# Performance work log

Hardware: AMD Instinct MI355X
Metric: run time of the kernel (lower is better)

Reference implementation:

```python
import jax, jax.numpy as jnp
import numpy as np

DIM = 192
HEADS = 6
HEAD_DIM = DIM // HEADS          # 32
N_WIN_TOK = 2 * 6 * 12           # 144 tokens per (2,6,12) window
BIAS_ROWS = (2 * 12 - 1) * 6 * 6 * 2 * 2  # 3312
N_WINDOWS = 960


def setup_inputs() -> dict:
    key = jax.random.key(0)
    ks = jax.random.split(key, 8)
    x = jax.random.normal(ks[0], (N_WINDOWS, N_WIN_TOK, DIM), dtype=jnp.float32)
    mask = jax.random.randint(ks[1], (N_WINDOWS, N_WIN_TOK, N_WIN_TOK), 0, 2, dtype=jnp.int32)
    rel_index = jax.random.randint(ks[2], (N_WIN_TOK, N_WIN_TOK), 0, BIAS_ROWS, dtype=jnp.int32)
    # parameters (torch nn.Linear equivalents, stored as [in, out])
    w_qkv = jax.random.normal(ks[3], (DIM, 3 * DIM), dtype=jnp.float32) * 0.02
    b_qkv = jnp.zeros((3 * DIM,), dtype=jnp.float32)
    w_out = jax.random.normal(ks[4], (DIM, DIM), dtype=jnp.float32) * 0.02
    b_out = jnp.zeros((DIM,), dtype=jnp.float32)
    bias_table = jax.random.normal(ks[5], (BIAS_ROWS, HEADS), dtype=jnp.float32) * 0.02
    return {"x": x, "mask": mask, "rel_index": rel_index,
            "w_qkv": w_qkv, "b_qkv": b_qkv, "w_out": w_out, "b_out": b_out,
            "bias_table": bias_table}


def reference(x, mask, rel_index, w_qkv, b_qkv, w_out, b_out, bias_table):
    nW, N, dim = x.shape
    scale = jnp.asarray(HEAD_DIM, x.dtype) ** -0.5
    # qkv projection: [nW, N, 3, heads, head_dim]
    qkv = (x @ w_qkv + b_qkv).reshape(nW, N, 3, HEADS, HEAD_DIM)
    q, k, v = qkv[:, :, 0], qkv[:, :, 1], qkv[:, :, 2]   # each [nW, N, heads, hd]
    # attention scores [nW, heads, N, N]
    attn = jnp.einsum('wnhd,wmhd->whnm', q * scale, k)
    # relative-position bias gather: table[rel_index] -> [N, N, heads] -> [heads, N, N]
    bias = bias_table[rel_index].transpose(2, 0, 1)
    attn = attn + bias[None]
    # additive mask: positions where mask == 0 get -1e9
    attn = jnp.where(mask[:, None, :, :] == 0, jnp.asarray(-1e9, attn.dtype), attn)
    attn = jax.nn.softmax(attn, axis=-1)
    out = jnp.einsum('whnm,wmhd->wnhd', attn, v).reshape(nW, N, dim)
    return out @ w_out + b_out
```

## Files before the change

### kernel.cpp

```cpp
#include <hip/hip_runtime.h>
#include <math.h>

#define NW 960
#define NT 144
#define DIM 192
#define NH 6
#define HD 32
#define WCOLS 576

typedef __bf16 bf16x8 __attribute__((ext_vector_type(8)));
typedef float floatx4 __attribute__((ext_vector_type(4)));

__device__ __forceinline__ unsigned short f2bf(float x) {
    union { float f; unsigned u; } v; v.f = x;
    unsigned r = v.u + 0x7fffu + ((v.u >> 16) & 1u);
    return (unsigned short)(r >> 16);
}
__device__ __forceinline__ float bf2f(unsigned short b) {
    union { unsigned u; float f; } v; v.u = ((unsigned)b) << 16;
    return v.f;
}
__device__ __forceinline__ floatx4 mfma16(bf16x8 a, bf16x8 b, floatx4 c) {
    return __builtin_amdgcn_mfma_f32_16x16x32_bf16(a, b, c, 0, 0, 0);
}
__device__ __forceinline__ bf16x8 lds_ld8(const unsigned short* p) {
    bf16x8 v;
    __builtin_memcpy(&v, p, 16);
    return v;
}

__global__ void prep_bias(const int* __restrict__ rel_index,
                          const float* __restrict__ bias_table,
                          float* __restrict__ bias_pre) {
    int i = blockIdx.x * 256 + threadIdx.x;
    if (i < NH * NT * NT) {
        int h = i / (NT * NT);
        int rem = i - h * (NT * NT);
        bias_pre[i] = bias_table[rel_index[rem] * NH + h];
    }
}

__global__ void prep_wq_frag(const float* __restrict__ w_qkv,
                             unsigned short* __restrict__ wh,
                             unsigned short* __restrict__ wl) {
    int i = blockIdx.x * 256 + threadIdx.x;
    if (i < NH * 6 * 6 * 512) {
        int h = i / 18432; int r = i - h * 18432;
        int j = r / 3072;  r -= j * 3072;
        int kt = r / 512;  r -= kt * 512;
        int lane = r >> 3, pos = r & 7;
        int col96 = j * 16 + (lane & 15);
        int k = kt * 32 + (lane >> 4) * 8 + pos;
        float v = w_qkv[k * WCOLS + (col96 >> 5) * DIM + h * HD + (col96 & 31)];
        unsigned short hi = f2bf(v);
        wh[i] = hi;
        wl[i] = f2bf(v - bf2f(hi));
    }
}

__global__ void prep_wo_frag(const float* __restrict__ w_out,
                             unsigned short* __restrict__ wh,
                             unsigned short* __restrict__ wl) {
    int i = blockIdx.x * 256 + threadIdx.x;
    if (i < 12 * 6 * 512) {
        int nt = i / 3072; int r = i - nt * 3072;
        int kt = r / 512;  r -= kt * 512;
        int lane = r >> 3, pos = r & 7;
        int ocol = nt * 16 + (lane & 15);
        int k = kt * 32 + (lane >> 4) * 8 + pos;
        float v = w_out[k * DIM + ocol];
        unsigned short hi = f2bf(v);
        wh[i] = hi;
        wl[i] = f2bf(v - bf2f(hi));
    }
}

__global__ __launch_bounds__(768, 3)
void fused(const float* __restrict__ x, const int* __restrict__ mask,
           const float* __restrict__ bias_pre,
           const unsigned short* __restrict__ wqh, const unsigned short* __restrict__ wql,
           const float* __restrict__ b_qkv,
           const unsigned short* __restrict__ woh_g, const unsigned short* __restrict__ wol_g,
           const float* __restrict__ b_out, float* __restrict__ out)
{
    __shared__ __align__(16) unsigned short lds[63904];
    const int XFo = 0, Q2o = 27648, K2o = 36864, V2o = 46080, Po = 56320, MBo = 62464;

    const int t = threadIdx.x;
    const int w = blockIdx.x;
    const int lane = t & 63, wv = t >> 6;
    const int c = lane & 15, q = lane >> 4;
    const float scale = 0.17677669529663687f;
    const float* xg = x + (size_t)w * NT * DIM;

    {
        unsigned* XFd = (unsigned*)&lds[XFo];
        #pragma unroll
        for (int l = 0; l < 18; ++l) {
            int d = t + l * 768;
            int kt = d / 2304; int r2 = d - kt * 2304;
            int tile = r2 >> 8; int r3 = r2 & 255;
            int ln = r3 >> 2, pp = r3 & 3;
            int n = tile * 16 + (ln & 15);
            int k = kt * 32 + (ln >> 4) * 8 + pp * 2;
            float2 xv = *(const float2*)&xg[n * DIM + k];
            XFd[d] = (unsigned)f2bf(xv.x) | ((unsigned)f2bf(xv.y) << 16);
        }
    }
    for (int e = t; e < 1024; e += 768) {
        int gi = e >> 8, l2 = 32 + ((e >> 3) & 31), pos = e & 7;
        lds[V2o + (gi * 5 + 4) * 512 + l2 * 8 + pos] = 0;
    }
    {
        unsigned* mb = (unsigned*)&lds[MBo];
        #pragma unroll 4
        for (int rr = 0; rr < 12; ++rr) {
            int n = wv * 12 + rr;
            const int* mrow = mask + ((size_t)w * NT + n) * NT;
            unsigned long long b0 = __ballot(mrow[lane] != 0);
            unsigned long long b1 = __ballot(mrow[64 + lane] != 0);
            int mv = (lane < 16) ? mrow[128 + lane] : 0;
            unsigned long long b2 = __ballot(mv != 0);
            if (lane == 0) {
                mb[n * 5 + 0] = (unsigned)b0;
                mb[n * 5 + 1] = (unsigned)(b0 >> 32);
                mb[n * 5 + 2] = (unsigned)b1;
                mb[n * 5 + 3] = (unsigned)(b1 >> 32);
                mb[n * 5 + 4] = (unsigned)b2;
            }
        }
    }

    const int hl   = wv / 6;
    const int j6   = wv % 6;
    const int part = j6 >> 1;
    const int jj   = j6 & 1;
    const int hl2  = wv & 1;
    const int sA   = wv >> 1;

    floatx4 Oacc[3][2][2];

    auto attn_unit = [&](int g, int s, floatx4* O) {
        const int hB = 2 * g + hl2;
        float bb[4][9];
        const float* bbase = bias_pre + hB * (NT * NT) + (s * 16 + q * 4) * NT + c;
        #pragma unroll
        for (int r = 0; r < 4; ++r)
            #pragma unroll
            for (int nt = 0; nt < 9; ++nt)
                bb[r][nt] = bbase[r * NT + nt * 16];
        bf16x8 qf = *(const bf16x8*)&lds[Q2o + (hl2 * 9 + s) * 512 + lane * 8];
        floatx4 sacc[9];
        __builtin_amdgcn_s_setprio(1);
        #pragma unroll
        for (int nt = 0; nt < 9; ++nt) {
            bf16x8 kf = *(const bf16x8*)&lds[K2o + (hl2 * 9 + nt) * 512 + lane * 8];
            sacc[nt] = mfma16(qf, kf, (floatx4)0.0f);
        }
        __builtin_amdgcn_s_setprio(0);
        const unsigned* mb = (const unsigned*)&lds[MBo];
        unsigned mwv[4][5];
        #pragma unroll
        for (int r = 0; r < 4; ++r) {
            int n = s * 16 + q * 4 + r;
            #pragma unroll
            for (int k5 = 0; k5 < 5; ++k5) mwv[r][k5] = mb[n * 5 + k5];
        }
        float e[4][9], mx[4];
        #pragma unroll
        for (int r = 0; r < 4; ++r) mx[r] = -1e30f;
        #pragma unroll
        for (int r = 0; r < 4; ++r)
            #pragma unroll
            for (int nt = 0; nt < 9; ++nt) {
                float val = sacc[nt][r] + bb[r][nt];
                unsigned bit = (mwv[r][nt >> 1] >> (((nt & 1) << 4) + c)) & 1u;
                val = bit ? val : -1e9f;
                e[r][nt] = val; mx[r] = fmaxf(mx[r], val);
            }
        #pragma unroll
        for (int o = 8; o; o >>= 1)
            #pragma unroll
            for (int r = 0; r < 4; ++r) mx[r] = fmaxf(mx[r], __shfl_xor(mx[r], o, 64));
        float sum[4] = {0.f, 0.f, 0.f, 0.f};
        #pragma unroll
        for (int r = 0; r < 4; ++r)
            #pragma unroll
            for (int nt = 0; nt < 9; ++nt) { e[r][nt] = __expf(e[r][nt] - mx[r]); sum[r] += e[r][nt]; }
        #pragma unroll
        for (int o = 8; o; o >>= 1)
            #pragma unroll
            for (int r = 0; r < 4; ++r) sum[r] += __shfl_xor(sum[r], o, 64);
        float rinv[4];
        #pragma unroll
        for (int r = 0; r < 4; ++r) rinv[r] = 1.0f / sum[r];
        floatx4 o0 = (floatx4)0.0f, o1 = (floatx4)0.0f;
        unsigned short* pbase = &lds[Po + wv * 512];
        #pragma unroll
        for (int sl = 0; sl < 5; ++sl) {
            asm volatile("" ::: "memory");
            #pragma unroll
            for (int r = 0; r < 4; ++r)
                #pragma unroll
                for (int ntl = 0; ntl < 2; ++ntl) {
                    int nt = 2 * sl + ntl;
                    unsigned short pv = 0;
                    if (nt < 9) pv = f2bf(e[r][nt] * rinv[r]);
                    pbase[((q * 4 + r) + 16 * ((ntl << 1) + (c >> 3))) * 8 + (c & 7)] = pv;
                }
            asm volatile("" ::: "memory");
            bf16x8 pf = lds_ld8(&pbase[lane * 8]);
            __builtin_amdgcn_s_setprio(1);
            o0 = mfma16(pf, *(const bf16x8*)&lds[V2o + ((hl2 * 2 + 0) * 5 + sl) * 512 + lane * 8], o0);
            o1 = mfma16(pf, *(const bf16x8*)&lds[V2o + ((hl2 * 2 + 1) * 5 + sl) * 512 + lane * 8], o1);
            __builtin_amdgcn_s_setprio(0);
        }
        O[0] = o0; O[1] = o1;
    };

    #pragma unroll
    for (int g = 0; g < 3; ++g) {
        __syncthreads();
        const int hg = 2 * g + hl;

        const unsigned short* bhp = wqh + (size_t)((hg * 6 + j6) * 6) * 512 + lane * 8;
        const unsigned short* blp = wql + (size_t)((hg * 6 + j6) * 6) * 512 + lane * 8;
        bf16x8 bh[6], bl[6];
        #pragma unroll
        for (int kt = 0; kt < 6; ++kt) {
            bh[kt] = *(const bf16x8*)&bhp[kt * 512];
            bl[kt] = *(const bf16x8*)&blp[kt * 512];
        }
        float bq = b_qkv[part * DIM + hg * HD + jj * 16 + c];

        #pragma unroll
        for (int i3 = 0; i3 < 3; ++i3) {
            floatx4 a[3];
            #pragma unroll
            for (int ii = 0; ii < 3; ++ii) a[ii] = (floatx4)0.0f;
            __builtin_amdgcn_s_setprio(1);
            #pragma unroll
            for (int kt = 0; kt < 6; ++kt) {
                #pragma unroll
                for (int ii = 0; ii < 3; ++ii) {
                    bf16x8 ah = *(const bf16x8*)&lds[XFo + (kt * 9 + i3 * 3 + ii) * 512 + lane * 8];
                    a[ii] = mfma16(ah, bh[kt], a[ii]);
                    a[ii] = mfma16(ah, bl[kt], a[ii]);
                }
            }
            __builtin_amdgcn_s_setprio(0);
            #pragma unroll
            for (int ii = 0; ii < 3; ++ii) {
                int i = i3 * 3 + ii;
                #pragma unroll
                for (int r = 0; r < 4; ++r) {
                    float v = a[ii][r] + bq;
                    int col32 = jj * 16 + c;
                    if (part == 0) {
                        lds[Q2o + (hl * 9 + i) * 512 + ((q * 4 + r) + 16 * (col32 >> 3)) * 8 + (col32 & 7)] = f2bf(v * scale);
                    } else if (part == 1) {
                        lds[K2o + (hl * 9 + i) * 512 + ((q * 4 + r) + 16 * (col32 >> 3)) * 8 + (col32 & 7)] = f2bf(v);
                    } else {
                        int n = i * 16 + q * 4 + r;
                        lds[V2o + ((hl * 2 + jj) * 5 + (n >> 5)) * 512 + (c + 16 * ((n >> 3) & 3)) * 8 + (n & 7)] = f2bf(v);
                    }
                }
            }
        }
        __syncthreads();

        attn_unit(g, sA, Oacc[g][0]);
        if (wv < 6) attn_unit(g, 6 + sA, Oacc[g][1]);
    }

    #pragma unroll
    for (int g = 0; g < 3; ++g) {
        int hB = 2 * g + hl2;
        #pragma unroll
        for (int ntv = 0; ntv < 2; ++ntv)
            #pragma unroll
            for (int r = 0; r < 4; ++r)
                lds[XFo + (hB * 9 + sA) * 512 +
                    ((q * 4 + r) + 16 * (ntv * 2 + (c >> 3))) * 8 + (c & 7)] =
                    f2bf(Oacc[g][0][ntv][r]);
        if (wv < 6) {
            #pragma unroll
            for (int ntv = 0; ntv < 2; ++ntv)
                #pragma unroll
                for (int r = 0; r < 4; ++r)
                    lds[XFo + (hB * 9 + 6 + sA) * 512 +
                        ((q * 4 + r) + 16 * (ntv * 2 + (c >> 3))) * 8 + (c & 7)] =
                        f2bf(Oacc[g][1][ntv][r]);
        }
    }
    __syncthreads();

    {
        const unsigned short* whp = woh_g + (size_t)(wv * 6) * 512 + lane * 8;
        const unsigned short* wlp = wol_g + (size_t)(wv * 6) * 512 + lane * 8;
        bf16x8 wh[6], wlo[6];
        #pragma unroll
        for (int kt = 0; kt < 6; ++kt) {
            wh[kt]  = *(const bf16x8*)&whp[kt * 512];
            wlo[kt] = *(const bf16x8*)&wlp[kt * 512];
        }
        float bo = b_out[wv * 16 + c];
        #pragma unroll
        for (int i3 = 0; i3 < 3; ++i3) {
            floatx4 a2[3];
            #pragma unroll
            for (int ii = 0; ii < 3; ++ii) a2[ii] = (floatx4)0.0f;
            __builtin_amdgcn_s_setprio(1);
            #pragma unroll
            for (int kt = 0; kt < 6; ++kt) {
                #pragma unroll
                for (int ii = 0; ii < 3; ++ii) {
                    bf16x8 af = *(const bf16x8*)&lds[XFo + (kt * 9 + i3 * 3 + ii) * 512 + lane * 8];
                    a2[ii] = mfma16(af, wh[kt], a2[ii]);
                    a2[ii] = mfma16(af, wlo[kt], a2[ii]);
                }
            }
            __builtin_amdgcn_s_setprio(0);
            #pragma unroll
            for (int ii = 0; ii < 3; ++ii) {
                int n0 = (i3 * 3 + ii) * 16 + q * 4;
                #pragma unroll
                for (int r = 0; r < 4; ++r) {
                    size_t ro = ((size_t)w * NT + n0 + r) * DIM;
                    out[ro + wv * 16 + c] = a2[ii][r] + bo;
                }
            }
        }
    }
}

__global__ __launch_bounds__(256, 2)
void attn_kernel(const float* __restrict__ x, const int* __restrict__ mask,
                 const int* __restrict__ rel_index, const float* __restrict__ w_qkv,
                 const float* __restrict__ b_qkv, const float* __restrict__ bias_table,
                 float* __restrict__ out)
{
    __shared__ float smem[19136];
    float* xt = smem;
    float* wt = smem + 4768;
    float* qs = smem;
    float* ks = smem + 4752;
    float* vs = smem + 9504;
    float* S  = smem + 14400;

    const int t  = threadIdx.x;
    const int w  = blockIdx.x / NH;
    const int h  = blockIdx.x % NH;
    const int tx = t & 15;
    const int ty = t >> 4;
    const float scale = 0.17677669529663687f;
    const float* xg = x + (size_t)w * NT * DIM;

    float acc[9][6];
    #pragma unroll
    for (int i = 0; i < 9; ++i)
        #pragma unroll
        for (int j = 0; j < 6; ++j) acc[i][j] = 0.f;

    for (int kt = 0; kt < 6; ++kt) {
        #pragma unroll
        for (int l = 0; l < 18; ++l) {
            int e = t + l * 256;
            int n = e >> 5, kk = e & 31;
            xt[kk * 149 + n] = xg[n * DIM + kt * 32 + kk];
        }
        #pragma unroll
        for (int l = 0; l < 12; ++l) {
            int e = t + l * 256;
            int kk = e / 96, cc = e - kk * 96;
            int col = (cc >> 5) * DIM + h * HD + (cc & 31);
            wt[kk * 96 + cc] = w_qkv[(kt * 32 + kk) * WCOLS + col];
        }
        __syncthreads();
        #pragma unroll
        for (int kk = 0; kk < 32; ++kk) {
            float a[9], b[6];
            #pragma unroll
            for (int i = 0; i < 9; ++i) a[i] = xt[kk * 149 + ty * 9 + i];
            #pragma unroll
            for (int j = 0; j < 6; ++j) b[j] = wt[kk * 96 + tx * 6 + j];
            #pragma unroll
            for (int i = 0; i < 9; ++i)
                #pragma unroll
                for (int j = 0; j < 6; ++j) acc[i][j] = fmaf(a[i], b[j], acc[i][j]);
        }
        __syncthreads();
    }

    #pragma unroll
    for (int j = 0; j < 6; ++j) {
        int cc = tx * 6 + j;
        int part = cc >> 5, jj = cc & 31;
        float bq = b_qkv[part * DIM + h * HD + jj];
        #pragma unroll
        for (int i = 0; i < 9; ++i) {
            int r = ty * 9 + i;
            float val = acc[i][j] + bq;
            if (part == 0)      qs[r * 33 + jj] = val * scale;
            else if (part == 1) ks[r * 33 + jj] = val;
            else                vs[r * 34 + jj] = val;
        }
    }
    __syncthreads();

    const int wave = t >> 6, lane = t & 63;
    for (int rt = 0; rt < 5; ++rt) {
        const int rows = (rt == 4) ? 16 : 32;
        {
            int r0 = ty * 2;
            int n0 = rt * 32 + r0; if (n0 > NT - 1) n0 = NT - 1;
            int n1 = n0 + 1;       if (n1 > NT - 1) n1 = NT - 1;
            int m0 = tx * 9;
            float s0[9], s1[9];
            #pragma unroll
            for (int j = 0; j < 9; ++j) { s0[j] = 0.f; s1[j] = 0.f; }
            #pragma unroll
            for (int kk = 0; kk < 32; ++kk) {
                float a0 = qs[n0 * 33 + kk];
                float a1 = qs[n1 * 33 + kk];
                #pragma unroll
                for (int j = 0; j < 9; ++j) {
                    float bk = ks[(m0 + j) * 33 + kk];
                    s0[j] = fmaf(a0, bk, s0[j]);
                    s1[j] = fmaf(a1, bk, s1[j]);
                }
            }
            if (r0 < rows) {
                #pragma unroll
                for (int j = 0; j < 9; ++j) S[r0 * 148 + m0 + j] = s0[j];
                #pragma unroll
                for (int j = 0; j < 9; ++j) S[(r0 + 1) * 148 + m0 + j] = s1[j];
            }
        }
        __syncthreads();

        for (int r = wave; r < rows; r += 4) {
            int n = rt * 32 + r;
            const int* mrow = mask + ((size_t)w * NT + n) * NT;
            const int* rrow = rel_index + n * NT;
            float e0 = S[r * 148 + lane] + bias_table[rrow[lane] * NH + h];
            if (mrow[lane] == 0) e0 = -1e9f;
            float e1 = S[r * 148 + 64 + lane] + bias_table[rrow[64 + lane] * NH + h];
            if (mrow[64 + lane] == 0) e1 = -1e9f;
            float e2 = -INFINITY;
            if (lane < 16) {
                e2 = S[r * 148 + 128 + lane] + bias_table[rrow[128 + lane] * NH + h];
                if (mrow[128 + lane] == 0) e2 = -1e9f;
            }
            float vmax = fmaxf(fmaxf(e0, e1), e2);
            #pragma unroll
            for (int off = 32; off > 0; off >>= 1)
                vmax = fmaxf(vmax, __shfl_xor(vmax, off, 64));
            float p0 = __expf(e0 - vmax);
            float p1 = __expf(e1 - vmax);
            float p2 = (lane < 16) ? __expf(e2 - vmax) : 0.f;
            float s = p0 + p1 + p2;
            #pragma unroll
            for (int off = 32; off > 0; off >>= 1)
                s += __shfl_xor(s, off, 64);
            float rinv = 1.f / s;
            S[r * 148 + lane] = p0 * rinv;
            S[r * 148 + 64 + lane] = p1 * rinv;
            if (lane < 16) S[r * 148 + 128 + lane] = p2 * rinv;
        }
        __syncthreads();

        {
            int r0 = ty * 2, dd0 = tx * 2;
            if (r0 < rows) {
                float o00 = 0, o01 = 0, o10 = 0, o11 = 0;
                #pragma unroll
                for (int m = 0; m < NT; ++m) {
                    float p0 = S[r0 * 148 + m];
                    float p1 = S[(r0 + 1) * 148 + m];
                    float2 vv = *(const float2*)&vs[m * 34 + dd0];
                    o00 = fmaf(p0, vv.x, o00);
                    o01 = fmaf(p0, vv.y, o01);
                    o10 = fmaf(p1, vv.x, o10);
                    o11 = fmaf(p1, vv.y, o11);
                }
                int n0 = rt * 32 + r0;
                *(float2*)&out[((size_t)(w * NT + n0)) * DIM + h * HD + dd0] = make_float2(o00, o01);
                *(float2*)&out[((size_t)(w * NT + n0 + 1)) * DIM + h * HD + dd0] = make_float2(o10, o11);
            }
        }
        __syncthreads();
    }
}

__global__ __launch_bounds__(256, 2)
void proj_kernel(float* __restrict__ io, const float* __restrict__ w_out,
                 const float* __restrict__ b_out)
{
    __shared__ float in_t[64 * 196];
    __shared__ float wt[32 * 192];
    const int t = threadIdx.x;
    const size_t row0 = (size_t)blockIdx.x * 64;

    #pragma unroll
    for (int l = 0; l < 12; ++l) {
        int e = t + l * 256;
        int r = e / 48, c4 = e - r * 48;
        float4 val = *(const float4*)&io[(row0 + r) * DIM + c4 * 4];
        *(float4*)&in_t[r * 196 + c4 * 4] = val;
    }
    const int tx = t & 15, ty = t >> 4;
    float acc[4][12];
    #pragma unroll
    for (int i = 0; i < 4; ++i)
        #pragma unroll
        for (int j = 0; j < 12; ++j) acc[i][j] = 0.f;

    for (int kt = 0; kt < 6; ++kt) {
        __syncthreads();
        #pragma unroll
        for (int l = 0; l < 6; ++l) {
            int e = t + l * 256;
            int kk = e / 48, c4 = e - kk * 48;
            *(float4*)&wt[kk * 192 + c4 * 4] =
                *(const float4*)&w_out[(kt * 32 + kk) * DIM + c4 * 4];
        }
        __syncthreads();
        #pragma unroll
        for (int kk = 0; kk < 32; ++kk) {
            float a[4];
            #pragma unroll
            for (int i = 0; i < 4; ++i) a[i] = in_t[(ty * 4 + i) * 196 + kt * 32 + kk];
            float b[12];
            #pragma unroll
            for (int j4 = 0; j4 < 3; ++j4) {
                float4 bb = *(const float4*)&wt[kk * 192 + tx * 12 + j4 * 4];
                b[j4 * 4] = bb.x; b[j4 * 4 + 1] = bb.y;
                b[j4 * 4 + 2] = bb.z; b[j4 * 4 + 3] = bb.w;
            }
            #pragma unroll
            for (int i = 0; i < 4; ++i)
                #pragma unroll
                for (int j = 0; j < 12; ++j)
                    acc[i][j] = fmaf(a[i], b[j], acc[i][j]);
        }
    }

    float bo[12];
    #pragma unroll
    for (int j4 = 0; j4 < 3; ++j4) {
        float4 bb = *(const float4*)&b_out[tx * 12 + j4 * 4];
        bo[j4 * 4] = bb.x; bo[j4 * 4 + 1] = bb.y;
        bo[j4 * 4 + 2] = bb.z; bo[j4 * 4 + 3] = bb.w;
    }
    #pragma unroll
    for (int i = 0; i < 4; ++i) {
        size_t r = row0 + ty * 4 + i;
        #pragma unroll
        for (int j4 = 0; j4 < 3; ++j4) {
            float4 o;
            o.x = acc[i][j4 * 4]     + bo[j4 * 4];
            o.y = acc[i][j4 * 4 + 1] + bo[j4 * 4 + 1];
            o.z = acc[i][j4 * 4 + 2] + bo[j4 * 4 + 2];
            o.w = acc[i][j4 * 4 + 3] + bo[j4 * 4 + 3];
            *(float4*)&io[r * DIM + tx * 12 + j4 * 4] = o;
        }
    }
}

extern "C" void kernel_launch(void* const* d_in, const int* in_sizes, int n_in,
                              void* d_out, int out_size, void* d_ws, size_t ws_size,
                              hipStream_t stream) {
    const float* x          = (const float*)d_in[0];
    const int*   mask       = (const int*)d_in[1];
    const int*   rel_index  = (const int*)d_in[2];
    const float* w_qkv      = (const float*)d_in[3];
    const float* b_qkv      = (const float*)d_in[4];
    const float* w_out      = (const float*)d_in[5];
    const float* b_out      = (const float*)d_in[6];
    const float* bias_table = (const float*)d_in[7];
    float* out = (float*)d_out;

    const size_t WS_NEED = 1087488;

    if (ws_size >= WS_NEED) {
        char* ws = (char*)d_ws;
        float*          bias_pre = (float*)ws;
        unsigned short* wq_h     = (unsigned short*)(ws + 497664);
        unsigned short* wq_l     = (unsigned short*)(ws + 718848);
        unsigned short* wo_h     = (unsigned short*)(ws + 940032);
        unsigned short* wo_l     = (unsigned short*)(ws + 1013760);

        hipLaunchKernelGGL(prep_bias, dim3(486), dim3(256), 0, stream,
                           rel_index, bias_table, bias_pre);
        hipLaunchKernelGGL(prep_wq_frag, dim3(432), dim3(256), 0, stream,
                           w_qkv, wq_h, wq_l);
        hipLaunchKernelGGL(prep_wo_frag, dim3(144), dim3(256), 0, stream,
                           w_out, wo_h, wo_l);
        hipLaunchKernelGGL(fused, dim3(NW), dim3(768), 0, stream,
                           x, mask, bias_pre, wq_h, wq_l, b_qkv,
                           wo_h, wo_l, b_out, out);
    } else {
        hipLaunchKernelGGL(attn_kernel, dim3(NW * NH), dim3(256), 0, stream,
                           x, mask, rel_index, w_qkv, b_qkv, bias_table, out);
        hipLaunchKernelGGL(proj_kernel, dim3(NW * NT / 64), dim3(256), 0, stream,
                           out, w_out, b_out);
    }
}
```

Baseline: 496.4 us.

## Pipeline per-head QKV projection with attention using double-buffered LDS

```diff
diff --git a/kernel.cpp b/kernel.cpp
--- a/kernel.cpp
+++ b/kernel.cpp
@@ -84,7 +84,10 @@
            const float* __restrict__ b_out, float* __restrict__ out)
 {
     __shared__ __align__(16) unsigned short lds[63904];
-    const int XFo = 0, Q2o = 27648, K2o = 36864, V2o = 46080, Po = 56320, MBo = 62464;
+    const int XFo = 0;
+    const int BUF0 = 27648, BUFSZ = 14336;
+    const int Q2off = 0, K2off = 4608, V2off = 9216;
+    const int Po = 56320, MBo = 62464;
 
     const int t = threadIdx.x;
     const int w = blockIdx.x;
@@ -108,8 +111,9 @@
         }
     }
     for (int e = t; e < 1024; e += 768) {
-        int gi = e >> 8, l2 = 32 + ((e >> 3) & 31), pos = e & 7;
-        lds[V2o + (gi * 5 + 4) * 512 + l2 * 8 + pos] = 0;
+        int b = e >> 9, r2 = e & 511;
+        int gi = r2 >> 8, l2 = 32 + ((r2 >> 3) & 31), pos = r2 & 7;
+        lds[BUF0 + b * BUFSZ + V2off + (gi * 5 + 4) * 512 + l2 * 8 + pos] = 0;
     }
     {
         unsigned* mb = (unsigned*)&lds[MBo];
@@ -131,30 +135,70 @@
         }
     }
 
-    const int hl   = wv / 6;
-    const int j6   = wv % 6;
-    const int part = j6 >> 1;
-    const int jj   = j6 & 1;
-    const int hl2  = wv & 1;
-    const int sA   = wv >> 1;
-
-    floatx4 Oacc[3][2][2];
-
-    auto attn_unit = [&](int g, int s, floatx4* O) {
-        const int hB = 2 * g + hl2;
+    auto qkv_tile = [&](int h, int j, int i3lo, int i3n) {
+        const int part = j >> 1, jj = j & 1;
+        unsigned short* buf = &lds[BUF0 + (h & 1) * BUFSZ];
+        const unsigned short* bhp = wqh + (size_t)((h * 6 + j) * 6) * 512 + lane * 8;
+        const unsigned short* blp = wql + (size_t)((h * 6 + j) * 6) * 512 + lane * 8;
+        bf16x8 bh[6], bl[6];
+        #pragma unroll
+        for (int kt = 0; kt < 6; ++kt) {
+            bh[kt] = *(const bf16x8*)&bhp[kt * 512];
+            bl[kt] = *(const bf16x8*)&blp[kt * 512];
+        }
+        float bq = b_qkv[part * DIM + h * HD + jj * 16 + c];
+        for (int i3x = 0; i3x < i3n; ++i3x) {
+            int i3 = i3lo + i3x;
+            floatx4 a[3];
+            #pragma unroll
+            for (int ii = 0; ii < 3; ++ii) a[ii] = (floatx4)0.0f;
+            __builtin_amdgcn_s_setprio(1);
+            #pragma unroll
+            for (int kt = 0; kt < 6; ++kt) {
+                #pragma unroll
+                for (int ii = 0; ii < 3; ++ii) {
+                    bf16x8 ah = *(const bf16x8*)&lds[XFo + (kt * 9 + i3 * 3 + ii) * 512 + lane * 8];
+                    a[ii] = mfma16(ah, bh[kt], a[ii]);
+                    a[ii] = mfma16(ah, bl[kt], a[ii]);
+                }
+            }
+            __builtin_amdgcn_s_setprio(0);
+            #pragma unroll
+            for (int ii = 0; ii < 3; ++ii) {
+                int i = i3 * 3 + ii;
+                #pragma unroll
+                for (int r = 0; r < 4; ++r) {
+                    float v = a[ii][r] + bq;
+                    int col32 = jj * 16 + c;
+                    if (part == 0) {
+                        buf[Q2off + i * 512 + ((q * 4 + r) + 16 * (col32 >> 3)) * 8 + (col32 & 7)] = f2bf(v * scale);
+                    } else if (part == 1) {
+                        buf[K2off + i * 512 + ((q * 4 + r) + 16 * (col32 >> 3)) * 8 + (col32 & 7)] = f2bf(v);
+                    } else {
+                        int n = i * 16 + q * 4 + r;
+                        buf[V2off + (jj * 5 + (n >> 5)) * 512 + (c + 16 * ((n >> 3) & 3)) * 8 + (n & 7)] = f2bf(v);
+                    }
+                }
+            }
+        }
+    };
+
+    auto attn_unit = [&](int h, floatx4 (&O)[2]) {
+        const int s = wv;
+        unsigned short* buf = &lds[BUF0 + (h & 1) * BUFSZ];
         float bb[4][9];
-        const float* bbase = bias_pre + hB * (NT * NT) + (s * 16 + q * 4) * NT + c;
+        const float* bbase = bias_pre + h * (NT * NT) + (s * 16 + q * 4) * NT + c;
         #pragma unroll
         for (int r = 0; r < 4; ++r)
             #pragma unroll
             for (int nt = 0; nt < 9; ++nt)
                 bb[r][nt] = bbase[r * NT + nt * 16];
-        bf16x8 qf = *(const bf16x8*)&lds[Q2o + (hl2 * 9 + s) * 512 + lane * 8];
+        bf16x8 qf = *(const bf16x8*)&buf[Q2off + s * 512 + lane * 8];
         floatx4 sacc[9];
         __builtin_amdgcn_s_setprio(1);
         #pragma unroll
         for (int nt = 0; nt < 9; ++nt) {
-            bf16x8 kf = *(const bf16x8*)&lds[K2o + (hl2 * 9 + nt) * 512 + lane * 8];
+            bf16x8 kf = *(const bf16x8*)&buf[K2off + nt * 512 + lane * 8];
             sacc[nt] = mfma16(qf, kf, (floatx4)0.0f);
         }
         __builtin_amdgcn_s_setprio(0);
@@ -211,87 +255,43 @@
             asm volatile("" ::: "memory");
             bf16x8 pf = lds_ld8(&pbase[lane * 8]);
             __builtin_amdgcn_s_setprio(1);
-            o0 = mfma16(pf, *(const bf16x8*)&lds[V2o + ((hl2 * 2 + 0) * 5 + sl) * 512 + lane * 8], o0);
-            o1 = mfma16(pf, *(const bf16x8*)&lds[V2o + ((hl2 * 2 + 1) * 5 + sl) * 512 + lane * 8], o1);
+            o0 = mfma16(pf, *(const bf16x8*)&buf[V2off + (0 * 5 + sl) * 512 + lane * 8], o0);
+            o1 = mfma16(pf, *(const bf16x8*)&buf[V2off + (1 * 5 + sl) * 512 + lane * 8], o1);
             __builtin_amdgcn_s_setprio(0);
         }
         O[0] = o0; O[1] = o1;
     };
 
+    floatx4 Oacc[6][2];
+
+    __syncthreads();
+
+    if (wv < 9) qkv_tile(0, wv / 3, wv % 3, 1);
+    else        qkv_tile(0, 3 + (wv - 9), 0, 3);
+
     #pragma unroll
-    for (int g = 0; g < 3; ++g) {
-        __syncthreads();
-        const int hg = 2 * g + hl;
-
-        const unsigned short* bhp = wqh + (size_t)((hg * 6 + j6) * 6) * 512 + lane * 8;
-        const unsigned short* blp = wql + (size_t)((hg * 6 + j6) * 6) * 512 + lane * 8;
-        bf16x8 bh[6], bl[6];
-        #pragma unroll
-        for (int kt = 0; kt < 6; ++kt) {
-            bh[kt] = *(const bf16x8*)&bhp[kt * 512];
-            bl[kt] = *(const bf16x8*)&blp[kt * 512];
-        }
-        float bq = b_qkv[part * DIM + hg * HD + jj * 16 + c];
-
-        #pragma unroll
-        for (int i3 = 0; i3 < 3; ++i3) {
-            floatx4 a[3];
-            #pragma unroll
-            for (int ii = 0; ii < 3; ++ii) a[ii] = (floatx4)0.0f;
-            __builtin_amdgcn_s_setprio(1);
-            #pragma unroll
-            for (int kt = 0; kt < 6; ++kt) {
-                #pragma unroll
-                for (int ii = 0; ii < 3; ++ii) {
-                    bf16x8 ah = *(const bf16x8*)&lds[XFo + (kt * 9 + i3 * 3 + ii) * 512 + lane * 8];
-                    a[ii] = mfma16(ah, bh[kt], a[ii]);
-                    a[ii] = mfma16(ah, bl[kt], a[ii]);
-                }
-            }
-            __builtin_amdgcn_s_setprio(0);
-            #pragma unroll
-            for (int ii = 0; ii < 3; ++ii) {
-                int i = i3 * 3 + ii;
-                #pragma unroll
-                for (int r = 0; r < 4; ++r) {
-                    float v = a[ii][r] + bq;
-                    int col32 = jj * 16 + c;
-                    if (part == 0) {
-                        lds[Q2o + (hl * 9 + i) * 512 + ((q * 4 + r) + 16 * (col32 >> 3)) * 8 + (col32 & 7)] = f2bf(v * scale);
-                    } else if (part == 1) {
-                        lds[K2o + (hl * 9 + i) * 512 + ((q * 4 + r) + 16 * (col32 >> 3)) * 8 + (col32 & 7)] = f2bf(v);
-                    } else {
-                        int n = i * 16 + q * 4 + r;
-                        lds[V2o + ((hl * 2 + jj) * 5 + (n >> 5)) * 512 + (c + 16 * ((n >> 3) & 3)) * 8 + (n & 7)] = f2bf(v);
-                    }
-                }
-            }
-        }
-        __syncthreads();
-
-        attn_unit(g, sA, Oacc[g][0]);
-        if (wv < 6) attn_unit(g, 6 + sA, Oacc[g][1]);
-    }
-
-    #pragma unroll
-    for (int g = 0; g < 3; ++g) {
-        int hB = 2 * g + hl2;
-        #pragma unroll
-        for (int ntv = 0; ntv < 2; ++ntv)
-            #pragma unroll
-            for (int r = 0; r < 4; ++r)
-                lds[XFo + (hB * 9 + sA) * 512 +
-                    ((q * 4 + r) + 16 * (ntv * 2 + (c >> 3))) * 8 + (c & 7)] =
-                    f2bf(Oacc[g][0][ntv][r]);
-        if (wv < 6) {
+    for (int h = 1; h < 6; ++h) {
+        __syncthreads();
+        if (wv < 9) {
+            attn_unit(h - 1, Oacc[h - 1]);
+            qkv_tile(h, wv / 3, wv % 3, 1);
+        } else {
+            qkv_tile(h, 3 + (wv - 9), 0, 3);
+        }
+    }
+
+    __syncthreads();
+    if (wv < 9) {
+        attn_unit(5, Oacc[5]);
+        #pragma unroll
+        for (int h = 0; h < 6; ++h)
             #pragma unroll
             for (int ntv = 0; ntv < 2; ++ntv)
                 #pragma unroll
                 for (int r = 0; r < 4; ++r)
-                    lds[XFo + (hB * 9 + 6 + sA) * 512 +
+                    lds[XFo + (h * 9 + wv) * 512 +
                         ((q * 4 + r) + 16 * (ntv * 2 + (c >> 3))) * 8 + (c & 7)] =
-                        f2bf(Oacc[g][1][ntv][r]);
-        }
+                        f2bf(Oacc[h][ntv][r]);
     }
     __syncthreads();
 
```

After: 451.5 us. 1.1x faster.
